# Kernel tuning notes

Hardware: AMD Instinct MI355X
Metric: run time of the kernel (lower is better)

The kernel has to match this reference:

```python
import jax, jax.numpy as jnp
import numpy as np
import math

EPS = 1e-5


def _layernorm(x, gamma, beta):
    mu = jnp.mean(x, axis=-1, keepdims=True)
    var = jnp.var(x, axis=-1, keepdims=True)
    return (x - mu) * jax.lax.rsqrt(var + EPS) * gamma + beta


def _quantum_head(x, theta_rx):
    # RX(x_i) then RX(theta_i) on wire i == RX(x_i + theta_i); product state,
    # CNOT ring is a Z-basis permutation => <Z_j> = prod_{i in S_j} cos(a_i)
    # with S_j = {0..j} for j>=1 (chain of CNOT(i,i+1)) and S_0 = {1..7}
    # (final CNOT(7,0) makes b0 = b1^...^b7).
    c = jnp.cos(x + theta_rx)                       # (B,S,8)
    cp = jnp.cumprod(c, axis=-1)                    # prefix products c0..cj
    z0 = jnp.prod(c[..., 1:], axis=-1, keepdims=True)
    return jnp.concatenate([z0, cp[..., 1:]], axis=-1)  # (B,S,8)


def _quantum_ffn(x, theta_ry):
    # RX(x_i) |0>, then RY(theta_i), measure Z: <Z_i> = cos(theta_i) * cos(x_i)
    return jnp.cos(theta_ry) * jnp.cos(x)


def setup_inputs() -> dict:
    key = jax.random.key(0)
    ks = jax.random.split(key, 6)
    B, S, E, F = 16, 2048, 8, 512
    return {
        'x': jax.random.normal(ks[0], (B, S, E), jnp.float32),
        'theta_rx': jax.random.normal(ks[1], (E,), jnp.float32),
        'w_out': jax.random.normal(ks[2], (E, E), jnp.float32) / math.sqrt(E),
        'theta_ry': jax.random.normal(ks[3], (E,), jnp.float32),
        'w1': jax.random.normal(ks[4], (F, E), jnp.float32) / math.sqrt(E),
        'b1': jnp.zeros((F,), jnp.float32),
        'w2': jax.random.normal(ks[5], (E, F), jnp.float32) / math.sqrt(F),
        'b2': jnp.zeros((E,), jnp.float32),
        'gamma1': jnp.ones((E,), jnp.float32),
        'beta1': jnp.zeros((E,), jnp.float32),
        'gamma2': jnp.ones((E,), jnp.float32),
        'beta2': jnp.zeros((E,), jnp.float32),
    }


def reference(x, theta_rx, w_out, theta_ry, w1, b1, w2, b2,
              gamma1, beta1, gamma2, beta2):
    B, S, E = x.shape
    H = 2
    D = E // H
    # --- quantum multi-head attention (shared head => q == k == v) ---
    z = _quantum_head(x, theta_rx)                       # (B,S,E)
    qh = z.reshape(B, S, H, D).transpose(0, 2, 1, 3)     # (B,H,S,D)
    scores = jnp.einsum('bhqd,bhkd->bhqk', qh, qh) / math.sqrt(D)
    attn = jax.nn.softmax(scores, axis=-1)
    out = jnp.einsum('bhqk,bhkd->bhqd', attn, qh)        # (B,H,S,D)
    out = out.transpose(0, 2, 1, 3).reshape(B, S, E)
    attn_out = out @ w_out.T                             # out_proj, no bias
    x1 = _layernorm(x + attn_out, gamma1, beta1)
    # --- quantum feed-forward ---
    zf = _quantum_ffn(x1, theta_ry)                      # (B,S,E)
    h = zf @ w1.T + b1                                   # (B,S,F)
    ffn_out = jax.nn.relu(h) @ w2.T + b2                 # (B,S,E)
    return _layernorm(x1 + ffn_out, gamma2, beta2)
```

## Files before the change

kernel.cpp:

```cpp
#include <hip/hip_runtime.h>
#include <math.h>
#include <utility>

#define NB 16
#define NS 2048
#define NE 8
#define NH 2
#define NF 512
#define DEG 6
#define NMONO 210
#define KPB 64
#define NCHUNK 32
#define PHI_LD 66
#define QPB 128
#define LNEPS 1e-5f
#define PART_STRIDE (5 * NMONO)

typedef float f32x2 __attribute__((ext_vector_type(2)));
typedef _Float16 h2 __attribute__((ext_vector_type(2)));

#if defined(__has_builtin)
# if __has_builtin(__builtin_amdgcn_fdot2)
#  define FDOT2(a,b,c) __builtin_amdgcn_fdot2((a),(b),(c),false)
# endif
#endif
#ifndef FDOT2
static __device__ __forceinline__ float fdot2_sw(h2 a, h2 b, float c) {
    return c + (float)a.x * (float)b.x + (float)a.y * (float)b.y;
}
# define FDOT2(a,b,c) fdot2_sw((a),(b),(c))
#endif

constexpr float ACOEF_C[7] = {0.99994459f, 2.00308514f, 2.00174650f,
                              1.30890404f, 0.65803033f, 0.31441604f, 0.10241921f};

constexpr int mono_e(int idx) {
    int i = 0;
    for (int e0 = 0; e0 <= DEG; ++e0)
        for (int e1 = 0; e1 <= DEG - e0; ++e1)
            for (int e2 = 0; e2 <= DEG - e0 - e1; ++e2)
                for (int e3 = 0; e3 <= DEG - e0 - e1 - e2; ++e3) {
                    if (i == idx) return (e0 << 12) | (e1 << 8) | (e2 << 4) | e3;
                    ++i;
                }
    return 0;
}
constexpr float mfact(int n) { float r = 1.f; for (int i = 2; i <= n; ++i) r *= (float)i; return r; }
constexpr float mono_c(int idx) {
    const int E = mono_e(idx);
    const int e0 = E >> 12, e1 = (E >> 8) & 15, e2 = (E >> 4) & 15, e3 = E & 15;
    const int d = e0 + e1 + e2 + e3;
    return ACOEF_C[d] * (mfact(d) / (mfact(e0) * mfact(e1) * mfact(e2) * mfact(e3)));
}

template <int BEG, class F, int... Is>
__device__ __forceinline__ void sf_impl(F f, std::integer_sequence<int, Is...>) {
    (f(std::integral_constant<int, BEG + Is>{}), ...);
}
template <int BEG, int END, class F>
__device__ __forceinline__ void static_for(F f) {
    sf_impl<BEG>(f, std::make_integer_sequence<int, END - BEG>{});
}

template <int BEG, int END>
__device__ __forceinline__ void phi_body(_Float16* __restrict__ Phi, int lane,
                                         const float (&pw0)[7], const float (&pw1)[7],
                                         const float (&pw2)[7], const float (&pw3)[7]) {
    static_for<BEG, END>([&](auto Ic) {
        constexpr int idx = Ic.value;
        constexpr int E = mono_e(idx);
        constexpr float C = mono_c(idx);
        const float v = C * (pw0[E >> 12] * pw1[(E >> 8) & 15]) *
                            (pw2[(E >> 4) & 15] * pw3[E & 15]);
        Phi[idx * PHI_LD + lane] = (_Float16)v;
    });
}

__global__ __launch_bounds__(256, 4)
void k1_moments(const float* __restrict__ x, const float* __restrict__ theta_rx,
                float* __restrict__ ws) {
    __shared__ _Float16 Phi[NMONO * PHI_LD];
    __shared__ __align__(16) _Float16 kvh[KPB / 2][8];
    __shared__ float th_s[8];

    const int t = threadIdx.x, bid = blockIdx.x;
    const int kc = bid & 31, h = (bid >> 5) & 1, b = bid >> 6;

    if (t < 8) th_s[t] = theta_rx[t];
    __syncthreads();

    const int lane = t & 63, wq = t >> 6;
    {
        const float* xr = x + ((size_t)b * NS + kc * KPB + lane) * NE;
        const float4 v0 = *reinterpret_cast<const float4*>(xr);
        const float4 v1 = *reinterpret_cast<const float4*>(xr + 4);
        const float c0 = __cosf(v0.x + th_s[0]), c1 = __cosf(v0.y + th_s[1]);
        const float c2 = __cosf(v0.z + th_s[2]), c3 = __cosf(v0.w + th_s[3]);
        const float c4 = __cosf(v1.x + th_s[4]), c5 = __cosf(v1.y + th_s[5]);
        const float c6 = __cosf(v1.z + th_s[6]), c7 = __cosf(v1.w + th_s[7]);
        const float p1 = c0*c1, p2 = p1*c2, p3 = p2*c3, p4 = p3*c4;
        const float p5 = p4*c5, p6 = p5*c6, p7 = p6*c7;
        float k0, k1v, k2v, k3v;
        if (h == 0) {
            const float s6 = c7*c6, s5 = s6*c5, s4 = s5*c4, s3 = s4*c3, s2 = s3*c2;
            k0 = s2*c1; k1v = p1; k2v = p2; k3v = p3;
        } else {
            k0 = p4; k1v = p5; k2v = p6; k3v = p7;
        }
        if (t < 64) {
            const int j = t >> 1, par = t & 1;
            kvh[j][0 + par] = (_Float16)k0;  kvh[j][2 + par] = (_Float16)k1v;
            kvh[j][4 + par] = (_Float16)k2v; kvh[j][6 + par] = (_Float16)k3v;
        }
        float pw0[7], pw1[7], pw2[7], pw3[7];
        pw0[0] = pw1[0] = pw2[0] = pw3[0] = 1.f;
        #pragma unroll
        for (int i = 1; i <= DEG; ++i) {
            pw0[i] = pw0[i-1] * k0;  pw1[i] = pw1[i-1] * k1v;
            pw2[i] = pw2[i-1] * k2v; pw3[i] = pw3[i-1] * k3v;
        }
        switch (wq) {
            case 0: phi_body<0,   53 >(Phi, lane, pw0, pw1, pw2, pw3); break;
            case 1: phi_body<53,  106>(Phi, lane, pw0, pw1, pw2, pw3); break;
            case 2: phi_body<106, 159>(Phi, lane, pw0, pw1, pw2, pw3); break;
            default: phi_body<159, 210>(Phi, lane, pw0, pw1, pw2, pw3); break;
        }
    }
    __syncthreads();

    if (t < NMONO) {
        const h2 one2 = {(_Float16)1.f, (_Float16)1.f};
        float a0 = 0.f, a1 = 0.f, a2 = 0.f, a3 = 0.f, a4 = 0.f;
        #pragma unroll 8
        for (int j = 0; j < KPB / 2; ++j) {
            const h2 phi2 = *reinterpret_cast<const h2*>(&Phi[t * PHI_LD + 2 * j]);
            const float4 kv4 = *reinterpret_cast<const float4*>(&kvh[j][0]);
            const h2 kA = __builtin_bit_cast(h2, kv4.x);
            const h2 kB = __builtin_bit_cast(h2, kv4.y);
            const h2 kC = __builtin_bit_cast(h2, kv4.z);
            const h2 kD = __builtin_bit_cast(h2, kv4.w);
            a0 = FDOT2(phi2, kA, a0);
            a1 = FDOT2(phi2, kB, a1);
            a2 = FDOT2(phi2, kC, a2);
            a3 = FDOT2(phi2, kD, a3);
            a4 = FDOT2(phi2, one2, a4);
        }
        float* dst = ws + (size_t)bid * PART_STRIDE;
        dst[0 * NMONO + t] = a0;
        dst[1 * NMONO + t] = a1;
        dst[2 * NMONO + t] = a2;
        dst[3 * NMONO + t] = a3;
        dst[4 * NMONO + t] = a4;
    }
}

template <int BEG, int END>
__device__ __forceinline__ void p2_body1(const float4* __restrict__ Mn,
                                         const float* __restrict__ Md, int base,
                                         const float (&pw)[4][7],
                                         f32x2& a01, f32x2& a23, float& ad) {
    static_for<BEG, END>([&](auto Ic) {
        constexpr int idx = Ic.value;
        constexpr int E = mono_e(idx);
        constexpr int e0 = E >> 12, e1 = (E >> 8) & 15, e2 = (E >> 4) & 15, e3 = E & 15;
        const float4 mv = Mn[base + idx];
        const float  md = Md[base + idx];
        const float P = (pw[0][e0] * pw[1][e1]) * (pw[2][e2] * pw[3][e3]);
        a01 += P * (f32x2){mv.x, mv.y};
        a23 += P * (f32x2){mv.z, mv.w};
        ad  += P * md;
    });
}

__global__ __launch_bounds__(1024, 4)
void k2_main(const float* __restrict__ x, const float* __restrict__ theta_rx,
             const float* __restrict__ w_out, const float* __restrict__ theta_ry,
             const float* __restrict__ w1, const float* __restrict__ b1,
             const float* __restrict__ w2, const float* __restrict__ b2,
             const float* __restrict__ g1, const float* __restrict__ be1,
             const float* __restrict__ g2, const float* __restrict__ be2,
             const float* __restrict__ ws, float* __restrict__ out) {
    __shared__ float4 Mn_lds[2 * NMONO];
    __shared__ float  Md_lds[2 * NMONO];
    __shared__ float  z_c[8][QPB];
    __shared__ float  x1_c[8][QPB];
    __shared__ float  zf_c[8][QPB];
    __shared__ float  attn_c[8][QPB];
    __shared__ float  part_a[4][256][5];
    __shared__ float  part_f[8][QPB][9];
    __shared__ float  w1_s[NF][NE];
    __shared__ float  w2t_s[NF][NE];
    __shared__ float  b1_s[NF];
    __shared__ float  wout_s[NE][NE];
    __shared__ float  th_s[8], cry_s[8], g1_s[8], be1_s[8], g2_s[8], be2_s[8], b2_s[8];

    const int t = threadIdx.x, bid = blockIdx.x;
    const int b = bid >> 4, qc = bid & 15;

    if (t < 2 * NMONO) {
        const int h = (t >= NMONO) ? 1 : 0;
        const int a = t - h * NMONO;
        const float* src = ws + (size_t)((b * 2 + h) * NCHUNK) * PART_STRIDE;
        float s0 = 0.f, s1 = 0.f, s2 = 0.f, s3 = 0.f, s4 = 0.f;
        #pragma unroll 4
        for (int kc = 0; kc < NCHUNK; ++kc) {
            const float* p = src + (size_t)kc * PART_STRIDE;
            s0 += p[0 * NMONO + a]; s1 += p[1 * NMONO + a];
            s2 += p[2 * NMONO + a]; s3 += p[3 * NMONO + a];
            s4 += p[4 * NMONO + a];
        }
        Mn_lds[t] = make_float4(s0, s1, s2, s3);
        Md_lds[t] = s4;
    }

    for (int i = t; i < NF * NE; i += 1024) {
        ((float*)w1_s)[i] = w1[i];
        const int e = i >> 9, f = i & (NF - 1);
        w2t_s[f][e] = w2[i];
    }
    if (t < NF) b1_s[t] = b1[t];
    if (t < NE * NE) ((float*)wout_s)[t] = w_out[t];
    if (t < 8) {
        th_s[t]  = theta_rx[t];
        cry_s[t] = __cosf(theta_ry[t]);
        g1_s[t]  = g1[t];  be1_s[t] = be1[t];
        g2_s[t]  = g2[t];  be2_s[t] = be2[t];
        b2_s[t]  = b2[t];
    }
    __syncthreads();

    if (t < QPB) {
        const float* xr = x + ((size_t)b * NS + qc * QPB + t) * NE;
        const float4 v0 = *reinterpret_cast<const float4*>(xr);
        const float4 v1 = *reinterpret_cast<const float4*>(xr + 4);
        const float c0 = __cosf(v0.x + th_s[0]), c1 = __cosf(v0.y + th_s[1]);
        const float c2 = __cosf(v0.z + th_s[2]), c3 = __cosf(v0.w + th_s[3]);
        const float c4 = __cosf(v1.x + th_s[4]), c5 = __cosf(v1.y + th_s[5]);
        const float c6 = __cosf(v1.z + th_s[6]), c7 = __cosf(v1.w + th_s[7]);
        const float p1 = c0*c1, p2 = p1*c2, p3 = p2*c3, p4 = p3*c4;
        const float p5 = p4*c5, p6 = p5*c6, p7 = p6*c7;
        const float s6 = c7*c6, s5 = s6*c5, s4 = s5*c4, s3 = s4*c3, s2 = s3*c2;
        z_c[0][t] = s2*c1; z_c[1][t] = p1; z_c[2][t] = p2; z_c[3][t] = p3;
        z_c[4][t] = p4;    z_c[5][t] = p5; z_c[6][t] = p6; z_c[7][t] = p7;
    }
    __syncthreads();

    {
        const int w = t >> 6, lane = t & 63;
        const int g = w & 3;
        const int h = (w >> 3) & 1;
        const int r = ((w >> 2) & 1) * 64 + lane;
        float pw[4][7];
        #pragma unroll
        for (int d = 0; d < 4; ++d) {
            const float u = z_c[h*4+d][r] * 0.25f;
            pw[d][0] = 1.f;
            #pragma unroll
            for (int i = 1; i <= DEG; ++i) pw[d][i] = pw[d][i-1] * u;
        }
        f32x2 a01 = {0.f,0.f}, a23 = {0.f,0.f};
        float ad = 0.f;
        const int base = h * NMONO;
        switch (g) {
            case 0: p2_body1<0,   53 >(Mn_lds, Md_lds, base, pw, a01, a23, ad); break;
            case 1: p2_body1<53,  106>(Mn_lds, Md_lds, base, pw, a01, a23, ad); break;
            case 2: p2_body1<106, 159>(Mn_lds, Md_lds, base, pw, a01, a23, ad); break;
            default: p2_body1<159, 210>(Mn_lds, Md_lds, base, pw, a01, a23, ad); break;
        }
        float* pa = &part_a[g][h * 128 + r][0];
        pa[0] = a01.x; pa[1] = a01.y; pa[2] = a23.x; pa[3] = a23.y; pa[4] = ad;
    }
    __syncthreads();

    if (t < 256) {
        const int h = t >> 7, r = t & 127;
        float n0 = 0.f, n1 = 0.f, n2 = 0.f, n3 = 0.f, dd = 0.f;
        #pragma unroll
        for (int g = 0; g < 4; ++g) {
            const float* pa = &part_a[g][t][0];
            n0 += pa[0]; n1 += pa[1]; n2 += pa[2]; n3 += pa[3]; dd += pa[4];
        }
        const float inv = 1.0f / dd;
        attn_c[h*4+0][r] = n0 * inv; attn_c[h*4+1][r] = n1 * inv;
        attn_c[h*4+2][r] = n2 * inv; attn_c[h*4+3][r] = n3 * inv;
    }
    __syncthreads();

    if (t < QPB) {
        float av[NE];
        #pragma unroll
        for (int e = 0; e < NE; ++e) av[e] = attn_c[e][t];
        float y[NE];
        #pragma unroll
        for (int e = 0; e < NE; ++e) {
            float acc = 0.f;
            #pragma unroll
            for (int k = 0; k < NE; ++k) acc += av[k] * wout_s[e][k];
            y[e] = acc;
        }
        const float* xr = x + ((size_t)b * NS + qc * QPB + t) * NE;
        const float4 xv0 = *reinterpret_cast<const float4*>(xr);
        const float4 xv1 = *reinterpret_cast<const float4*>(xr + 4);
        float t1[NE];
        t1[0] = xv0.x + y[0]; t1[1] = xv0.y + y[1]; t1[2] = xv0.z + y[2]; t1[3] = xv0.w + y[3];
        t1[4] = xv1.x + y[4]; t1[5] = xv1.y + y[5]; t1[6] = xv1.z + y[6]; t1[7] = xv1.w + y[7];
        float mu = 0.f;
        #pragma unroll
        for (int e = 0; e < NE; ++e) mu += t1[e];
        mu *= 0.125f;
        float var = 0.f;
        #pragma unroll
        for (int e = 0; e < NE; ++e) { const float d = t1[e] - mu; var += d * d; }
        var *= 0.125f;
        const float inv1 = rsqrtf(var + LNEPS);
        #pragma unroll
        for (int e = 0; e < NE; ++e) {
            const float x1e = (t1[e] - mu) * inv1 * g1_s[e] + be1_s[e];
            x1_c[e][t] = x1e;
            zf_c[e][t] = cry_s[e] * __cosf(x1e);
        }
    }
    __syncthreads();

    if (t < 256) {
        const int fs = t >> 5;
        const int rr = t & 31;
        f32x2 zf01[4], zf23[4], zf45[4], zf67[4];
        #pragma unroll
        for (int k = 0; k < 4; ++k) {
            const int row = rr + 32 * k;
            zf01[k] = (f32x2){zf_c[0][row], zf_c[1][row]};
            zf23[k] = (f32x2){zf_c[2][row], zf_c[3][row]};
            zf45[k] = (f32x2){zf_c[4][row], zf_c[5][row]};
            zf67[k] = (f32x2){zf_c[6][row], zf_c[7][row]};
        }
        f32x2 a01[4] = {}, a23[4] = {}, a45[4] = {}, a67[4] = {};
        #pragma unroll 4
        for (int i = 0; i < 64; ++i) {
            const int f = fs * 64 + i;
            const float4 wa = *reinterpret_cast<const float4*>(&w1_s[f][0]);
            const float4 wb = *reinterpret_cast<const float4*>(&w1_s[f][4]);
            const float bb = b1_s[f];
            const float4 ua = *reinterpret_cast<const float4*>(&w2t_s[f][0]);
            const float4 ub = *reinterpret_cast<const float4*>(&w2t_s[f][4]);
            const f32x2 wa01 = {wa.x, wa.y}, wa23 = {wa.z, wa.w};
            const f32x2 wb45 = {wb.x, wb.y}, wb67 = {wb.z, wb.w};
            const f32x2 ua01 = {ua.x, ua.y}, ua23 = {ua.z, ua.w};
            const f32x2 ub45 = {ub.x, ub.y}, ub67 = {ub.z, ub.w};
            #pragma unroll
            for (int k = 0; k < 4; ++k) {
                const f32x2 ha = zf01[k] * wa01 + zf23[k] * wa23;
                const f32x2 hb = zf45[k] * wb45 + zf67[k] * wb67;
                float hv = bb + ha.x + ha.y + hb.x + hb.y;
                hv = fmaxf(hv, 0.f);
                a01[k] += hv * ua01;  a23[k] += hv * ua23;
                a45[k] += hv * ub45;  a67[k] += hv * ub67;
            }
        }
        #pragma unroll
        for (int k = 0; k < 4; ++k) {
            const int row = rr + 32 * k;
            float* pf = &part_f[fs][row][0];
            pf[0] = a01[k].x; pf[1] = a01[k].y; pf[2] = a23[k].x; pf[3] = a23[k].y;
            pf[4] = a45[k].x; pf[5] = a45[k].y; pf[6] = a67[k].x; pf[7] = a67[k].y;
        }
    }
    __syncthreads();

    {
        const int e = t >> 7, r = t & 127;
        float s = 0.f;
        #pragma unroll
        for (int fs = 0; fs < 8; ++fs) s += part_f[fs][r][e];
        zf_c[e][r] = x1_c[e][r] + s + b2_s[e];
    }
    __syncthreads();

    if (t < QPB) {
        float t2[NE];
        #pragma unroll
        for (int e = 0; e < NE; ++e) t2[e] = zf_c[e][t];
        float mu = 0.f;
        #pragma unroll
        for (int e = 0; e < NE; ++e) mu += t2[e];
        mu *= 0.125f;
        float var = 0.f;
        #pragma unroll
        for (int e = 0; e < NE; ++e) { const float d = t2[e] - mu; var += d * d; }
        var *= 0.125f;
        const float inv2 = rsqrtf(var + LNEPS);
        float o[NE];
        #pragma unroll
        for (int e = 0; e < NE; ++e) o[e] = (t2[e] - mu) * inv2 * g2_s[e] + be2_s[e];
        float4* o4 = reinterpret_cast<float4*>(out + ((size_t)b * NS + qc * QPB + t) * NE);
        o4[0] = make_float4(o[0], o[1], o[2], o[3]);
        o4[1] = make_float4(o[4], o[5], o[6], o[7]);
    }
}

extern "C" void kernel_launch(void* const* d_in, const int* in_sizes, int n_in,
                              void* d_out, int out_size, void* d_ws, size_t ws_size,
                              hipStream_t stream) {
    const float* x        = (const float*)d_in[0];
    const float* theta_rx = (const float*)d_in[1];
    const float* w_out    = (const float*)d_in[2];
    const float* theta_ry = (const float*)d_in[3];
    const float* w1       = (const float*)d_in[4];
    const float* b1       = (const float*)d_in[5];
    const float* w2       = (const float*)d_in[6];
    const float* b2       = (const float*)d_in[7];
    const float* g1       = (const float*)d_in[8];
    const float* be1      = (const float*)d_in[9];
    const float* g2       = (const float*)d_in[10];
    const float* be2      = (const float*)d_in[11];
    float* out = (float*)d_out;
    float* ws  = (float*)d_ws;

    k1_moments<<<dim3(NB * NH * NCHUNK), dim3(256), 0, stream>>>(x, theta_rx, ws);
    k2_main<<<dim3(NB * (NS / QPB)), dim3(1024), 0, stream>>>(
        x, theta_rx, w_out, theta_ry, w1, b1, w2, b2, g1, be1, g2, be2, ws, out);
}
```

Baseline: 35.87 us.

## Spread FFN across all 1024 threads with shuffle reduction and remap block indices

The feed-forward stage now uses all 1024 threads: each group of 8 lanes handles one row, and each lane takes an interleaved eighth of the hidden units. Partial sums are combined with xor-shuffles instead of an LDS partial buffer, which removes two barriers and a reduction pass, and the final layernorm output is written one element per lane. The block-to-(batch, chunk) mapping is also changed so that neighbouring blocks work on different batches, which may change how workspace reads spread across the device. In exchange, each lane now redoes the full 8-wide dot product and the layernorm statistics, and the output is written as scalar stores.

Result: faster. 33.03 us (-7.9%).

```diff
diff --git a/kernel.cpp b/kernel.cpp
--- a/kernel.cpp
+++ b/kernel.cpp
@@ -187,7 +187,6 @@
     __shared__ float  zf_c[8][QPB];
     __shared__ float  attn_c[8][QPB];
     __shared__ float  part_a[4][256][5];
-    __shared__ float  part_f[8][QPB][9];
     __shared__ float  w1_s[NF][NE];
     __shared__ float  w2t_s[NF][NE];
     __shared__ float  b1_s[NF];
@@ -195,7 +194,8 @@
     __shared__ float  th_s[8], cry_s[8], g1_s[8], be1_s[8], g2_s[8], be2_s[8], b2_s[8];
 
     const int t = threadIdx.x, bid = blockIdx.x;
-    const int b = bid >> 4, qc = bid & 15;
+    const int b  = (bid & 7) + 8 * ((bid >> 3) & 1);
+    const int qc = bid >> 4;
 
     if (t < 2 * NMONO) {
         const int h = (t >= NMONO) ? 1 : 0;
@@ -322,64 +322,36 @@
     }
     __syncthreads();
 
-    if (t < 256) {
-        const int fs = t >> 5;
-        const int rr = t & 31;
-        f32x2 zf01[4], zf23[4], zf45[4], zf67[4];
-        #pragma unroll
-        for (int k = 0; k < 4; ++k) {
-            const int row = rr + 32 * k;
-            zf01[k] = (f32x2){zf_c[0][row], zf_c[1][row]};
-            zf23[k] = (f32x2){zf_c[2][row], zf_c[3][row]};
-            zf45[k] = (f32x2){zf_c[4][row], zf_c[5][row]};
-            zf67[k] = (f32x2){zf_c[6][row], zf_c[7][row]};
-        }
-        f32x2 a01[4] = {}, a23[4] = {}, a45[4] = {}, a67[4] = {};
-        #pragma unroll 4
+    {
+        const int r = t >> 3, sub = t & 7;
+        float zf[NE];
+        #pragma unroll
+        for (int e = 0; e < NE; ++e) zf[e] = zf_c[e][r];
+        f32x2 a01 = {0.f,0.f}, a23 = {0.f,0.f}, a45 = {0.f,0.f}, a67 = {0.f,0.f};
+        #pragma unroll 8
         for (int i = 0; i < 64; ++i) {
-            const int f = fs * 64 + i;
+            const int f = sub + (i << 3);
             const float4 wa = *reinterpret_cast<const float4*>(&w1_s[f][0]);
             const float4 wb = *reinterpret_cast<const float4*>(&w1_s[f][4]);
-            const float bb = b1_s[f];
+            float hv = b1_s[f] + zf[0]*wa.x + zf[1]*wa.y + zf[2]*wa.z + zf[3]*wa.w
+                               + zf[4]*wb.x + zf[5]*wb.y + zf[6]*wb.z + zf[7]*wb.w;
+            hv = fmaxf(hv, 0.f);
             const float4 ua = *reinterpret_cast<const float4*>(&w2t_s[f][0]);
             const float4 ub = *reinterpret_cast<const float4*>(&w2t_s[f][4]);
-            const f32x2 wa01 = {wa.x, wa.y}, wa23 = {wa.z, wa.w};
-            const f32x2 wb45 = {wb.x, wb.y}, wb67 = {wb.z, wb.w};
-            const f32x2 ua01 = {ua.x, ua.y}, ua23 = {ua.z, ua.w};
-            const f32x2 ub45 = {ub.x, ub.y}, ub67 = {ub.z, ub.w};
+            a01 += hv * (f32x2){ua.x, ua.y};
+            a23 += hv * (f32x2){ua.z, ua.w};
+            a45 += hv * (f32x2){ub.x, ub.y};
+            a67 += hv * (f32x2){ub.z, ub.w};
+        }
+        float acc[NE] = {a01.x, a01.y, a23.x, a23.y, a45.x, a45.y, a67.x, a67.y};
+        #pragma unroll
+        for (int m = 1; m < 8; m <<= 1) {
             #pragma unroll
-            for (int k = 0; k < 4; ++k) {
-                const f32x2 ha = zf01[k] * wa01 + zf23[k] * wa23;
-                const f32x2 hb = zf45[k] * wb45 + zf67[k] * wb67;
-                float hv = bb + ha.x + ha.y + hb.x + hb.y;
-                hv = fmaxf(hv, 0.f);
-                a01[k] += hv * ua01;  a23[k] += hv * ua23;
-                a45[k] += hv * ub45;  a67[k] += hv * ub67;
-            }
-        }
-        #pragma unroll
-        for (int k = 0; k < 4; ++k) {
-            const int row = rr + 32 * k;
-            float* pf = &part_f[fs][row][0];
-            pf[0] = a01[k].x; pf[1] = a01[k].y; pf[2] = a23[k].x; pf[3] = a23[k].y;
-            pf[4] = a45[k].x; pf[5] = a45[k].y; pf[6] = a67[k].x; pf[7] = a67[k].y;
-        }
-    }
-    __syncthreads();
-
-    {
-        const int e = t >> 7, r = t & 127;
-        float s = 0.f;
-        #pragma unroll
-        for (int fs = 0; fs < 8; ++fs) s += part_f[fs][r][e];
-        zf_c[e][r] = x1_c[e][r] + s + b2_s[e];
-    }
-    __syncthreads();
-
-    if (t < QPB) {
+            for (int e = 0; e < NE; ++e) acc[e] += __shfl_xor(acc[e], m, 64);
+        }
         float t2[NE];
         #pragma unroll
-        for (int e = 0; e < NE; ++e) t2[e] = zf_c[e][t];
+        for (int e = 0; e < NE; ++e) t2[e] = x1_c[e][r] + acc[e] + b2_s[e];
         float mu = 0.f;
         #pragma unroll
         for (int e = 0; e < NE; ++e) mu += t2[e];
@@ -389,12 +361,8 @@
         for (int e = 0; e < NE; ++e) { const float d = t2[e] - mu; var += d * d; }
         var *= 0.125f;
         const float inv2 = rsqrtf(var + LNEPS);
-        float o[NE];
-        #pragma unroll
-        for (int e = 0; e < NE; ++e) o[e] = (t2[e] - mu) * inv2 * g2_s[e] + be2_s[e];
-        float4* o4 = reinterpret_cast<float4*>(out + ((size_t)b * NS + qc * QPB + t) * NE);
-        o4[0] = make_float4(o[0], o[1], o[2], o[3]);
-        o4[1] = make_float4(o[4], o[5], o[6], o[7]);
+        out[((size_t)b * NS + qc * QPB + r) * NE + sub] =
+            (t2[sub] - mu) * inv2 * g2_s[sub] + be2_s[sub];
     }
 }
 
```
